# Optimization experiments

Measured on AMD Instinct MI355X. Metric: run time of the kernel, lower is better.

## Reference

```python
import jax, jax.numpy as jnp
import numpy as np

IN_FEATURES = 1024
OUT_FEATURES = 1024
BATCH = 32
SEQ = 1024
EPS = 1e-8


def setup_inputs() -> dict:
    key = jax.random.key(0)
    k1, k2, k3 = jax.random.split(key, 3)
    Efou = jax.random.normal(k1, (BATCH, SEQ, IN_FEATURES), dtype=jnp.float32)
    y = jax.random.normal(k2, (BATCH, IN_FEATURES), dtype=jnp.float32)
    weight = jax.random.normal(k3, (IN_FEATURES, OUT_FEATURES), dtype=jnp.float32)
    return {"Efou": Efou, "y": y, "weight": weight}


def reference(Efou, y, weight):
    # scale = 1/sqrt(in_features)
    scale = 1.0 / np.sqrt(np.float32(weight.shape[0]))
    ys = y * scale  # (b, i) == per-sample column scaling of weight
    # Demodulation norm: sum_i (scale*W[i,o]*y[b,i])^2 = (ys^2) @ (W^2)
    d = jax.lax.rsqrt(jnp.einsum('bi,io->bo', ys * ys, weight * weight) + EPS)  # (b, o)
    # Efou @ (scale*W*y*d) == ((Efou*ys) @ W) * d  -- same math, avoids (b,i,o) weight
    out = jnp.einsum('bsi,io->bso', Efou * ys[:, None, :], weight) * d[:, None, :]
    return out
```

## Files before the change

kernel.cpp:

```cpp
#include <hip/hip_runtime.h>

#define AS1 __attribute__((address_space(1)))
#define AS3 __attribute__((address_space(3)))

typedef __bf16 bf16x8 __attribute__((ext_vector_type(8)));
typedef float f32x4 __attribute__((ext_vector_type(4)));

__device__ __forceinline__ unsigned short f2bf(float f) {
  union { float f; unsigned u; } v; v.f = f;
  unsigned u = v.u;
  unsigned r = (u + 0x7fffu + ((u >> 16) & 1u)) >> 16;
  return (unsigned short)r;
}

__global__ __launch_bounds__(256) void dcalc_a_kernel(const float* __restrict__ y,
                                                      const float* __restrict__ W,
                                                      float* __restrict__ partial) {
  __shared__ float ysq[32][32];
  const int o = blockIdx.x * 256 + threadIdx.x;
  const int i0 = blockIdx.y * 32;
  for (int e = threadIdx.x; e < 1024; e += 256) {
    int il = e >> 5, b = e & 31;
    float t = y[b * 1024 + i0 + il] * 0.03125f;
    ysq[il][b] = t * t;
  }
  __syncthreads();

  f32x4 acc[8] = {};
#pragma unroll
  for (int il = 0; il < 32; ++il) {
    float w = W[(size_t)(i0 + il) * 1024 + o];
    float w2 = w * w;
#pragma unroll
    for (int b4 = 0; b4 < 8; ++b4) {
      f32x4 q = *(const f32x4*)&ysq[il][b4 * 4];
#pragma unroll
      for (int k = 0; k < 4; ++k) acc[b4][k] = fmaf(q[k], w2, acc[b4][k]);
    }
  }
  float* p = partial + (size_t)blockIdx.y * 32768 + o;
#pragma unroll
  for (int b4 = 0; b4 < 8; ++b4)
#pragma unroll
    for (int k = 0; k < 4; ++k) p[(b4 * 4 + k) * 1024] = acc[b4][k];
}

__global__ __launch_bounds__(256) void dcalc_b_kernel(const float* __restrict__ partial,
                                                      float* __restrict__ dmod) {
  const int bo = blockIdx.x * 256 + threadIdx.x;
  float acc = 0.f;
#pragma unroll 8
  for (int is = 0; is < 32; ++is) acc += partial[(size_t)is * 32768 + bo];
  dmod[bo] = rsqrtf(acc + 1e-8f);
}

__global__ void wconv_kernel(const float* __restrict__ W,
                             unsigned short* __restrict__ WT) {
  __shared__ float t[32][33];
  const int tx = threadIdx.x;
  const int ty = threadIdx.y;
  const int i0 = blockIdx.y * 32;
  const int o0 = blockIdx.x * 32;
#pragma unroll
  for (int k = 0; k < 4; ++k)
    t[ty + k * 8][tx] = W[(size_t)(i0 + ty + k * 8) * 1024 + o0 + tx];
  __syncthreads();
#pragma unroll
  for (int k = 0; k < 4; ++k)
    WT[(size_t)(o0 + ty + k * 8) * 1024 + i0 + tx] = f2bf(t[tx][ty + k * 8]);
}

__global__ __launch_bounds__(256) void xconv_kernel(const float4* __restrict__ E4,
                                                    const float* __restrict__ y,
                                                    unsigned short* __restrict__ X) {
  const size_t total = (size_t)8388608;
  for (size_t g = (size_t)blockIdx.x * blockDim.x + threadIdx.x; g < total;
       g += (size_t)gridDim.x * blockDim.x) {
    float4 v = E4[g];
    size_t e = g * 4;
    int i = (int)(e & 1023);
    int b = (int)(e >> 20);
    float4 yv = *(const float4*)(y + b * 1024 + i);
    ushort4 o;
    o.x = f2bf(v.x * yv.x * 0.03125f);
    o.y = f2bf(v.y * yv.y * 0.03125f);
    o.z = f2bf(v.z * yv.z * 0.03125f);
    o.w = f2bf(v.w * yv.w * 0.03125f);
    *(ushort4*)(X + e) = o;
  }
}

#define NT 16
#define LDS_TILE 65536

#define BAR __builtin_amdgcn_s_barrier()
#define LGKM0 asm volatile("s_waitcnt lgkmcnt(0)" ::: "memory")
#define VM(n) asm volatile("s_waitcnt vmcnt(" #n ")" ::: "memory")
#define SCHB __builtin_amdgcn_sched_barrier(0)
#define PRIO(x) __builtin_amdgcn_s_setprio(x)

#define STG_A(r, t, dst)                                                     \
  __builtin_amdgcn_global_load_lds(                                          \
      (const AS1 void*)(Xs + (size_t)(r) * 64 * 2048 + (t) * 128),           \
      (AS3 void*)((dst) + (r) * 8192 + sldso), 16, 0, 0)
#define STG_B(r, t, dst)                                                     \
  __builtin_amdgcn_global_load_lds(                                          \
      (const AS1 void*)(Ws + (size_t)(r) * 64 * 2048 + (t) * 128),           \
      (AS3 void*)((dst) + 32768 + (r) * 8192 + sldso), 16, 0, 0)

#define RD_A(mh, mi, kk)                                                     \
  (*(const bf16x8*)(Ab + (wr * 128 + ((mh) * 4 + (mi)) * 16 + l15) * 128 +   \
                    ((((kk) * 64 + lhi * 16)) ^ swz_rd)))
#define RD_B(nh, ni, kk)                                                     \
  (*(const bf16x8*)(Bb + (wc * 64 + ((nh) * 2 + (ni)) * 16 + l15) * 128 +    \
                    ((((kk) * 64 + lhi * 16)) ^ swz_rd)))

#define LD_A(mh)                                                             \
  { _Pragma("unroll") for (int mi = 0; mi < 4; ++mi)                         \
      _Pragma("unroll") for (int kk = 0; kk < 2; ++kk)                       \
        a[mi][kk] = RD_A(mh, mi, kk); }
#define LD_B(nh)                                                             \
  { _Pragma("unroll") for (int ni = 0; ni < 2; ++ni)                         \
      _Pragma("unroll") for (int kk = 0; kk < 2; ++kk)                       \
        bfr[ni][kk] = RD_B(nh, ni, kk); }

#define MM(mh, nh)                                                           \
  do {                                                                       \
    _Pragma("unroll") for (int mi = 0; mi < 4; ++mi)                         \
      _Pragma("unroll") for (int ni = 0; ni < 2; ++ni)                       \
        _Pragma("unroll") for (int kk = 0; kk < 2; ++kk)                     \
          acc[(mh) * 4 + mi][(nh) * 2 + ni] =                                \
              __builtin_amdgcn_mfma_f32_16x16x32_bf16(                       \
                  a[mi][kk], bfr[ni][kk], acc[(mh) * 4 + mi][(nh) * 2 + ni], \
                  0, 0, 0);                                                  \
  } while (0)

__global__ __launch_bounds__(512, 2) void gemm8d_kernel(
    const unsigned short* __restrict__ X, const unsigned short* __restrict__ WT,
    const float* __restrict__ dmod, float* __restrict__ out) {
  extern __shared__ char lds[];
  const int tid = threadIdx.x;
  const int bid = blockIdx.x;
  const int wg = (bid & 7) * 64 + (bid >> 3);
  const int bm = wg >> 2, bn = wg & 3;
  const int m0 = bm * 256, n0 = bn * 256;

  const int w = tid >> 6, l = tid & 63;
  const int wr = w >> 2, wc = w & 3;
  const int l15 = l & 15, lhi = l >> 4;
  const int swz_rd = (l15 & 7) << 4;

  const int srow = tid >> 3;
  const int scb = ((tid & 7) << 4) ^ ((srow & 7) << 4);
  const char* Xs = (const char*)X + (size_t)(m0 + srow) * 2048 + scb;
  const char* Ws = (const char*)WT + (size_t)(n0 + srow) * 2048 + scb;
  const int sldso = tid * 16;

  f32x4 acc[8][4] = {};
  bf16x8 a[4][2], bfr[2][2];

  char* buf0 = lds;
  char* buf1 = lds + LDS_TILE;

  STG_A(0, 0, buf0); STG_A(2, 0, buf0); STG_A(1, 0, buf0); STG_A(3, 0, buf0);
  STG_B(0, 0, buf0); STG_B(1, 0, buf0); STG_B(2, 0, buf0); STG_B(3, 0, buf0);
  STG_A(0, 1, buf1); STG_A(2, 1, buf1); STG_A(1, 1, buf1); STG_A(3, 1, buf1);
  VM(4);
  BAR;

  for (int t = 0; t < NT - 2; ++t) {
    const char* Ab = lds + (t & 1) * LDS_TILE;
    const char* Bb = Ab + 32768;
    char* dB = lds + ((t + 1) & 1) * LDS_TILE;
    char* dA = lds + (t & 1) * LDS_TILE;
    const int t1 = t + 1, t2 = t + 2;
    const bool stA = (t2 < NT);
    LD_A(0); LD_B(0);
    STG_B(0, t1, dB); STG_B(1, t1, dB);
    BAR; LGKM0; SCHB; PRIO(1); MM(0, 0); PRIO(0); SCHB; BAR;
    LD_B(1);
    STG_B(2, t1, dB); STG_B(3, t1, dB);
    BAR; LGKM0; SCHB; PRIO(1); MM(0, 1); PRIO(0); SCHB; BAR;
    LD_A(1); LD_B(0);
    if (stA) { STG_A(0, t2, dA); STG_A(2, t2, dA); }
    BAR; LGKM0; SCHB; PRIO(1); MM(1, 0); PRIO(0); SCHB; BAR;
    LD_B(1);
    if (stA) { STG_A(1, t2, dA); STG_A(3, t2, dA); }
    BAR; LGKM0; SCHB; PRIO(1); MM(1, 1); PRIO(0); SCHB;
    VM(4);
    BAR;
  }

  {
    const int t = NT - 2;
    const char* Ab = lds + (t & 1) * LDS_TILE;
    const char* Bb = Ab + 32768;
    char* dB = lds + ((t + 1) & 1) * LDS_TILE;
    const int t1 = t + 1;
    LD_A(0); LD_B(0);
    STG_B(0, t1, dB); STG_B(1, t1, dB);
    BAR; LGKM0; SCHB; PRIO(1); MM(0, 0); PRIO(0); SCHB; BAR;
    LD_B(1);
    STG_B(2, t1, dB); STG_B(3, t1, dB);
    BAR; LGKM0; SCHB; PRIO(1); MM(0, 1); PRIO(0); SCHB; BAR;
    LD_A(1); LD_B(0);
    BAR; LGKM0; SCHB; PRIO(1); MM(1, 0); PRIO(0); SCHB; BAR;
    LD_B(1);
    BAR; LGKM0; SCHB; PRIO(1); MM(1, 1); PRIO(0); SCHB;
    VM(0);
    BAR;
  }

  {
    const char* Ab = lds + ((NT - 1) & 1) * LDS_TILE;
    const char* Bb = Ab + 32768;
    LD_A(0); LD_B(0);
    BAR; LGKM0; SCHB; PRIO(1); MM(0, 0); PRIO(0); SCHB; BAR;
    LD_B(1);
    BAR; LGKM0; SCHB; PRIO(1); MM(0, 1); PRIO(0); SCHB; BAR;
    LD_A(1); LD_B(0);
    BAR; LGKM0; SCHB; PRIO(1); MM(1, 0); PRIO(0); SCHB; BAR;
    LD_B(1);
    BAR; LGKM0; SCHB; PRIO(1); MM(1, 1); PRIO(0); SCHB;
  }

  const int b = m0 >> 10;
  const int col0 = n0 + wc * 64 + l15;
  float dv[4];
#pragma unroll
  for (int nf = 0; nf < 4; ++nf) dv[nf] = dmod[b * 1024 + col0 + nf * 16];
#pragma unroll
  for (int mf = 0; mf < 8; ++mf) {
#pragma unroll
    for (int j = 0; j < 4; ++j) {
      const int row = m0 + wr * 128 + mf * 16 + lhi * 4 + j;
      float* orow = out + (size_t)row * 1024 + col0;
#pragma unroll
      for (int nf = 0; nf < 4; ++nf) orow[nf * 16] = acc[mf][nf][j] * dv[nf];
    }
  }
}

extern "C" void kernel_launch(void* const* d_in, const int* in_sizes, int n_in,
                              void* d_out, int out_size, void* d_ws, size_t ws_size,
                              hipStream_t stream) {
  const float* Efou = (const float*)d_in[0];
  const float* y    = (const float*)d_in[1];
  const float* W    = (const float*)d_in[2];
  float* out = (float*)d_out;

  unsigned short* X  = (unsigned short*)d_ws;
  unsigned short* WT = X + (size_t)32768 * 1024;
  float* dmod        = (float*)(WT + (size_t)1024 * 1024);
  float* dpart       = dmod + 32768;

  hipFuncSetAttribute((const void*)gemm8d_kernel,
                      hipFuncAttributeMaxDynamicSharedMemorySize, 131072);

  dcalc_a_kernel<<<dim3(4, 32), 256, 0, stream>>>(y, W, dpart);
  dcalc_b_kernel<<<128, 256, 0, stream>>>(dpart, dmod);
  wconv_kernel<<<dim3(32, 32), dim3(32, 8), 0, stream>>>(W, WT);
  xconv_kernel<<<2048, 256, 0, stream>>>((const float4*)Efou, y, X);
  gemm8d_kernel<<<512, 512, 131072, stream>>>(X, WT, dmod, out);
}
```

Measured before the change: 138.6 us.

## Fold weight bf16 transpose into dcalc and demod reduction into GEMM prologue

The bf16 conversion and transpose of W now happen inside the demodulation partial-sum kernel, which already reads W. Each thread packs its 32 bf16 values and writes them with vector stores, so the separate wconv kernel goes away. The dcalc_b reduction kernel is also removed: each GEMM block sums the 32 partials for its 256 columns into an LDS table before its main loop. This drops two kernel launches and one pass over W, at the cost of a short serial prologue in every GEMM block and a slightly larger LDS allocation.

New measurement: 135.1 us. 1.03x faster.

```diff
diff --git a/kernel.cpp b/kernel.cpp
--- a/kernel.cpp
+++ b/kernel.cpp
@@ -5,6 +5,7 @@
 
 typedef __bf16 bf16x8 __attribute__((ext_vector_type(8)));
 typedef float f32x4 __attribute__((ext_vector_type(4)));
+typedef unsigned short ushort8 __attribute__((ext_vector_type(8)));
 
 __device__ __forceinline__ unsigned short f2bf(float f) {
   union { float f; unsigned u; } v; v.f = f;
@@ -13,9 +14,10 @@
   return (unsigned short)r;
 }
 
-__global__ __launch_bounds__(256) void dcalc_a_kernel(const float* __restrict__ y,
-                                                      const float* __restrict__ W,
-                                                      float* __restrict__ partial) {
+__global__ __launch_bounds__(256) void prep_kernel(const float* __restrict__ y,
+                                                   const float* __restrict__ W,
+                                                   float* __restrict__ partial,
+                                                   unsigned short* __restrict__ WT) {
   __shared__ float ysq[32][32];
   const int o = blockIdx.x * 256 + threadIdx.x;
   const int i0 = blockIdx.y * 32;
@@ -27,9 +29,11 @@
   __syncthreads();
 
   f32x4 acc[8] = {};
+  ushort8 wb[4];
 #pragma unroll
   for (int il = 0; il < 32; ++il) {
     float w = W[(size_t)(i0 + il) * 1024 + o];
+    wb[il >> 3][il & 7] = f2bf(w);
     float w2 = w * w;
 #pragma unroll
     for (int b4 = 0; b4 < 8; ++b4) {
@@ -38,36 +42,14 @@
       for (int k = 0; k < 4; ++k) acc[b4][k] = fmaf(q[k], w2, acc[b4][k]);
     }
   }
+  unsigned short* wt = WT + (size_t)o * 1024 + i0;
+#pragma unroll
+  for (int q = 0; q < 4; ++q) *(ushort8*)(wt + q * 8) = wb[q];
   float* p = partial + (size_t)blockIdx.y * 32768 + o;
 #pragma unroll
   for (int b4 = 0; b4 < 8; ++b4)
 #pragma unroll
     for (int k = 0; k < 4; ++k) p[(b4 * 4 + k) * 1024] = acc[b4][k];
-}
-
-__global__ __launch_bounds__(256) void dcalc_b_kernel(const float* __restrict__ partial,
-                                                      float* __restrict__ dmod) {
-  const int bo = blockIdx.x * 256 + threadIdx.x;
-  float acc = 0.f;
-#pragma unroll 8
-  for (int is = 0; is < 32; ++is) acc += partial[(size_t)is * 32768 + bo];
-  dmod[bo] = rsqrtf(acc + 1e-8f);
-}
-
-__global__ void wconv_kernel(const float* __restrict__ W,
-                             unsigned short* __restrict__ WT) {
-  __shared__ float t[32][33];
-  const int tx = threadIdx.x;
-  const int ty = threadIdx.y;
-  const int i0 = blockIdx.y * 32;
-  const int o0 = blockIdx.x * 32;
-#pragma unroll
-  for (int k = 0; k < 4; ++k)
-    t[ty + k * 8][tx] = W[(size_t)(i0 + ty + k * 8) * 1024 + o0 + tx];
-  __syncthreads();
-#pragma unroll
-  for (int k = 0; k < 4; ++k)
-    WT[(size_t)(o0 + ty + k * 8) * 1024 + i0 + tx] = f2bf(t[tx][ty + k * 8]);
 }
 
 __global__ __launch_bounds__(256) void xconv_kernel(const float4* __restrict__ E4,
@@ -137,13 +119,16 @@
 
 __global__ __launch_bounds__(512, 2) void gemm8d_kernel(
     const unsigned short* __restrict__ X, const unsigned short* __restrict__ WT,
-    const float* __restrict__ dmod, float* __restrict__ out) {
+    const float* __restrict__ dpart, float* __restrict__ out) {
   extern __shared__ char lds[];
+  float* dtab = (float*)(lds + 2 * LDS_TILE);
+
   const int tid = threadIdx.x;
   const int bid = blockIdx.x;
   const int wg = (bid & 7) * 64 + (bid >> 3);
   const int bm = wg >> 2, bn = wg & 3;
   const int m0 = bm * 256, n0 = bn * 256;
+  const int b = m0 >> 10;
 
   const int w = tid >> 6, l = tid & 63;
   const int wr = w >> 2, wc = w & 3;
@@ -161,6 +146,15 @@
 
   char* buf0 = lds;
   char* buf1 = lds + LDS_TILE;
+
+  if (tid < 256) {
+    const float* dp = dpart + b * 1024 + n0 + tid;
+    float s = 0.f;
+#pragma unroll 8
+    for (int is = 0; is < 32; ++is) s += dp[(size_t)is * 32768];
+    dtab[tid] = rsqrtf(s + 1e-8f);
+  }
+  __syncthreads();
 
   STG_A(0, 0, buf0); STG_A(2, 0, buf0); STG_A(1, 0, buf0); STG_A(3, 0, buf0);
   STG_B(0, 0, buf0); STG_B(1, 0, buf0); STG_B(2, 0, buf0); STG_B(3, 0, buf0);
@@ -174,7 +168,6 @@
     char* dB = lds + ((t + 1) & 1) * LDS_TILE;
     char* dA = lds + (t & 1) * LDS_TILE;
     const int t1 = t + 1, t2 = t + 2;
-    const bool stA = (t2 < NT);
     LD_A(0); LD_B(0);
     STG_B(0, t1, dB); STG_B(1, t1, dB);
     BAR; LGKM0; SCHB; PRIO(1); MM(0, 0); PRIO(0); SCHB; BAR;
@@ -182,10 +175,10 @@
     STG_B(2, t1, dB); STG_B(3, t1, dB);
     BAR; LGKM0; SCHB; PRIO(1); MM(0, 1); PRIO(0); SCHB; BAR;
     LD_A(1); LD_B(0);
-    if (stA) { STG_A(0, t2, dA); STG_A(2, t2, dA); }
+    STG_A(0, t2, dA); STG_A(2, t2, dA);
     BAR; LGKM0; SCHB; PRIO(1); MM(1, 0); PRIO(0); SCHB; BAR;
     LD_B(1);
-    if (stA) { STG_A(1, t2, dA); STG_A(3, t2, dA); }
+    STG_A(1, t2, dA); STG_A(3, t2, dA);
     BAR; LGKM0; SCHB; PRIO(1); MM(1, 1); PRIO(0); SCHB;
     VM(4);
     BAR;
@@ -224,17 +217,16 @@
     BAR; LGKM0; SCHB; PRIO(1); MM(1, 1); PRIO(0); SCHB;
   }
 
-  const int b = m0 >> 10;
-  const int col0 = n0 + wc * 64 + l15;
+  const int lc0 = wc * 64 + l15;
   float dv[4];
 #pragma unroll
-  for (int nf = 0; nf < 4; ++nf) dv[nf] = dmod[b * 1024 + col0 + nf * 16];
+  for (int nf = 0; nf < 4; ++nf) dv[nf] = dtab[lc0 + nf * 16];
 #pragma unroll
   for (int mf = 0; mf < 8; ++mf) {
 #pragma unroll
     for (int j = 0; j < 4; ++j) {
       const int row = m0 + wr * 128 + mf * 16 + lhi * 4 + j;
-      float* orow = out + (size_t)row * 1024 + col0;
+      float* orow = out + (size_t)row * 1024 + n0 + lc0;
 #pragma unroll
       for (int nf = 0; nf < 4; ++nf) orow[nf * 16] = acc[mf][nf][j] * dv[nf];
     }
@@ -251,15 +243,12 @@
 
   unsigned short* X  = (unsigned short*)d_ws;
   unsigned short* WT = X + (size_t)32768 * 1024;
-  float* dmod        = (float*)(WT + (size_t)1024 * 1024);
-  float* dpart       = dmod + 32768;
+  float* dpart       = (float*)(WT + (size_t)1024 * 1024);
 
   hipFuncSetAttribute((const void*)gemm8d_kernel,
-                      hipFuncAttributeMaxDynamicSharedMemorySize, 131072);
-
-  dcalc_a_kernel<<<dim3(4, 32), 256, 0, stream>>>(y, W, dpart);
-  dcalc_b_kernel<<<128, 256, 0, stream>>>(dpart, dmod);
-  wconv_kernel<<<dim3(32, 32), dim3(32, 8), 0, stream>>>(W, WT);
+                      hipFuncAttributeMaxDynamicSharedMemorySize, 132096);
+
+  prep_kernel<<<dim3(4, 32), 256, 0, stream>>>(y, W, dpart, WT);
   xconv_kernel<<<2048, 256, 0, stream>>>((const float4*)Efou, y, X);
-  gemm8d_kernel<<<512, 512, 131072, stream>>>(X, WT, dmod, out);
-}
+  gemm8d_kernel<<<512, 512, 132096, stream>>>(X, WT, dpart, out);
+}
```
